# Kernel tuning notes

Hardware: AMD Instinct MI355X
Metric: run time of the kernel (lower is better)

The kernel has to match this reference:

```python
import jax, jax.numpy as jnp
import numpy as np

def setup_inputs() -> dict:
    key = jax.random.key(0)
    ks = jax.random.split(key, 8)
    B, n, in_dim, h = 4, 512, 300, 128
    word_vecs = jax.random.normal(ks[0], (B, n, in_dim), dtype=jnp.float32)
    mask = jnp.zeros((B, n, h), dtype=jnp.float32)
    s_in = 1.0 / np.sqrt(in_dim)
    s_h = 1.0 / np.sqrt(h)
    Wx_w = jax.random.normal(ks[1], (h, in_dim), dtype=jnp.float32) * s_in
    Wx_b = jnp.zeros((h,), dtype=jnp.float32)
    Wa_w = jax.random.normal(ks[2], (h, h), dtype=jnp.float32) * s_h
    Wa_b = jnp.zeros((h,), dtype=jnp.float32)
    Ua_w = jax.random.normal(ks[3], (h, h), dtype=jnp.float32) * s_h
    Ua_b = jnp.zeros((h,), dtype=jnp.float32)
    return {"word_vecs": word_vecs, "mask": mask, "Wx_w": Wx_w, "Wx_b": Wx_b,
            "Wa_w": Wa_w, "Wa_b": Wa_b, "Ua_w": Ua_w, "Ua_b": Ua_b}

def reference(word_vecs, mask, Wx_w, Wx_b, Wa_w, Wa_b, Ua_w, Ua_b):
    # h_vecs: [B, n, h]  (dropout layers are identity in eval mode)
    h_vecs = jnp.tanh(jnp.einsum('bni,hi->bnh', word_vecs, Wx_w) + Wx_b)
    ta = jnp.einsum('bnh,gh->bng', h_vecs, Wa_w) + Wa_b  # [B,n,h]
    tb = jnp.einsum('bnh,gh->bng', h_vecs, Ua_w) + Ua_b  # [B,n,h]
    # additive per-channel scores: [B, q, k, h]
    temp = jax.nn.elu(ta[:, :, None, :] + tb[:, None, :, :])
    a = jax.nn.softmax(temp + mask[:, None, :, :], axis=2)
    # weighted sum over keys: [B, q, h]
    c_vecs = jnp.einsum('bqkh,bkh->bqh', a, h_vecs)
    return c_vecs
```

## Files before the change

kernel.cpp:

```cpp
#include <hip/hip_runtime.h>

#define B_    4
#define N_    512
#define IND_  300
#define H_    128
#define QQ    8
#define KC    8
#define LOG2E 1.4426950408889634f

__global__ void pack_all(const float* __restrict__ Wx_w,
                         const float* __restrict__ Wa_w,
                         const float* __restrict__ Ua_w,
                         float* __restrict__ WxT4,
                         float* __restrict__ WaT4,
                         float* __restrict__ UaT4) {
    const int blk = blockIdx.x;
    const int t   = threadIdx.x;
    if (blk < IND_) {
        const int i = blk;
        WxT4[(i >> 2) * 512 + t * 4 + (i & 3)] = Wx_w[t * IND_ + i];
    } else if (blk < IND_ + H_) {
        const int i = blk - IND_;
        WaT4[(i >> 2) * 512 + t * 4 + (i & 3)] = Wa_w[t * H_ + i] * LOG2E;
    } else {
        const int i = blk - IND_ - H_;
        UaT4[(i >> 2) * 512 + t * 4 + (i & 3)] = Ua_w[t * H_ + i] * LOG2E;
    }
}

__global__ __launch_bounds__(128) void prep3(
    const float* __restrict__ x,
    const float* __restrict__ WxT4,
    const float* __restrict__ Wx_b,
    const float* __restrict__ WaT4,
    const float* __restrict__ Wa_b,
    const float* __restrict__ UaT4,
    const float* __restrict__ Ua_b,
    const float* __restrict__ mask,
    float* __restrict__ Eta,
    float4* __restrict__ kv)
{
    __shared__ __align__(16) float xs[304];
    __shared__ __align__(16) float hs[H_];

    const int r = blockIdx.x;
    const int t = threadIdx.x;

    const float* xrow = x + (size_t)r * IND_;
    for (int i = t; i < IND_; i += 128) xs[i] = xrow[i];
    __syncthreads();

    const float4* w4 = (const float4*)WxT4 + t;
    float acc = Wx_b[t];
    #pragma unroll 5
    for (int i4 = 0; i4 < IND_ / 4; ++i4) {
        float4 w  = w4[i4 * 128];
        float4 xv = *(const float4*)(xs + 4 * i4);
        acc = fmaf(w.x, xv.x, acc);
        acc = fmaf(w.y, xv.y, acc);
        acc = fmaf(w.z, xv.z, acc);
        acc = fmaf(w.w, xv.w, acc);
    }
    float h = tanhf(acc);
    hs[t] = h;
    __syncthreads();

    const float4* wa4 = (const float4*)WaT4 + t;
    const float4* ua4 = (const float4*)UaT4 + t;
    float accA = Wa_b[t] * LOG2E;
    float accU = Ua_b[t] * LOG2E;
    #pragma unroll 8
    for (int i4 = 0; i4 < H_ / 4; ++i4) {
        float4 wa = wa4[i4 * 128];
        float4 ua = ua4[i4 * 128];
        float4 hv = *(const float4*)(hs + 4 * i4);
        accA = fmaf(wa.x, hv.x, accA);
        accA = fmaf(wa.y, hv.y, accA);
        accA = fmaf(wa.z, hv.z, accA);
        accA = fmaf(wa.w, hv.w, accA);
        accU = fmaf(ua.x, hv.x, accU);
        accU = fmaf(ua.y, hv.y, accU);
        accU = fmaf(ua.z, hv.z, accU);
        accU = fmaf(ua.w, hv.w, accU);
    }
    const size_t o = (size_t)r * H_ + t;
    Eta[o] = __builtin_amdgcn_exp2f(accA);
    float M = __builtin_amdgcn_exp2f(mask[o] * LOG2E);
    kv[o]  = make_float4(__builtin_amdgcn_exp2f(accU), M, h, 0.f);
}

__global__ __launch_bounds__(128) void attn3(
    const float* __restrict__ Eta,
    const float4* __restrict__ kv,
    float2* __restrict__ accum)
{
    const int c  = blockIdx.x;
    const int qg = blockIdx.y;
    const int b  = blockIdx.z;
    const int h  = threadIdx.x;
    const int q0 = qg * QQ;
    const int k0 = c * (N_ / KC);

    float eta[QQ], l[QQ], cc[QQ];
    #pragma unroll
    for (int j = 0; j < QQ; ++j) {
        eta[j] = Eta[((size_t)(b * N_ + q0 + j)) * H_ + h];
        l[j] = 0.f;
        cc[j] = 0.f;
    }

    const float4* kp = kv + ((size_t)(b * N_ + k0)) * H_ + h;

    #pragma unroll 4
    for (int k = 0; k < N_ / KC; ++k) {
        float4 v = kp[(size_t)k * H_];
        #pragma unroll
        for (int j = 0; j < QQ; ++j) {
            float e  = eta[j] * v.x;
            float pn = __builtin_amdgcn_exp2f(fmaf(e, LOG2E, -LOG2E));
            float p0 = (e > 1.f) ? e : pn;
            float p  = p0 * v.y;
            l[j] += p;
            cc[j] = fmaf(p, v.z, cc[j]);
        }
    }

    #pragma unroll
    for (int j = 0; j < QQ; ++j) {
        accum[((size_t)c * (B_ * N_) + b * N_ + q0 + j) * H_ + h] =
            make_float2(l[j], cc[j]);
    }
}

__global__ void fin3(const float2* __restrict__ accum, float* __restrict__ out) {
    const int idx = blockIdx.x * 256 + threadIdx.x;
    float L = 0.f, C = 0.f;
    #pragma unroll
    for (int c = 0; c < KC; ++c) {
        float2 a = accum[(size_t)c * (B_ * N_ * H_) + idx];
        L += a.x;
        C += a.y;
    }
    out[idx] = C / L;
}

extern "C" void kernel_launch(void* const* d_in, const int* in_sizes, int n_in,
                              void* d_out, int out_size, void* d_ws, size_t ws_size,
                              hipStream_t stream) {
    const float* word_vecs = (const float*)d_in[0];
    const float* mask      = (const float*)d_in[1];
    const float* Wx_w      = (const float*)d_in[2];
    const float* Wx_b      = (const float*)d_in[3];
    const float* Wa_w      = (const float*)d_in[4];
    const float* Wa_b      = (const float*)d_in[5];
    const float* Ua_w      = (const float*)d_in[6];
    const float* Ua_b      = (const float*)d_in[7];
    float* out = (float*)d_out;

    char* p = (char*)d_ws;
    float*  WxT4  = (float*)p;   p += (size_t)75 * 512 * 4;
    float*  WaT4  = (float*)p;   p += (size_t)32 * 512 * 4;
    float*  UaT4  = (float*)p;   p += (size_t)32 * 512 * 4;
    float*  Eta   = (float*)p;   p += (size_t)B_ * N_ * H_ * 4;
    float4* kv    = (float4*)p;  p += (size_t)B_ * N_ * H_ * 16;
    float2* accum = (float2*)p;  p += (size_t)KC * B_ * N_ * H_ * 8;

    pack_all<<<IND_ + 2 * H_, 128, 0, stream>>>(Wx_w, Wa_w, Ua_w, WxT4, WaT4, UaT4);

    prep3<<<B_ * N_, 128, 0, stream>>>(word_vecs, WxT4, Wx_b,
                                       WaT4, Wa_b, UaT4, Ua_b,
                                       mask, Eta, kv);

    dim3 grid(KC, N_ / QQ, B_);
    attn3<<<grid, 128, 0, stream>>>(Eta, kv, accum);

    fin3<<<(B_ * N_ * H_) / 256, 256, 0, stream>>>(accum, out);
}
```

Measured before the change: 131.4 us.

## Process four rows per prep block, split keys finer, premultiply mask into values

The projection kernel now computes four rows per block, so each weight load is reused across rows and the x tile is loaded with float4. The key dimension is split into 16 chunks instead of 8 to create more attention blocks. The mask factor is folded into the stored value (M*h), so the inner loop uses two FMAs instead of a multiply plus add and FMA. The cost is a partial-sum buffer twice as large and more reduction traffic in the final kernel.

```diff
diff --git a/kernel.cpp b/kernel.cpp
--- a/kernel.cpp
+++ b/kernel.cpp
@@ -5,7 +5,8 @@
 #define IND_  300
 #define H_    128
 #define QQ    8
-#define KC    8
+#define KC    16
+#define RR    4
 #define LOG2E 1.4426950408889634f
 
 __global__ void pack_all(const float* __restrict__ Wx_w,
@@ -28,7 +29,7 @@
     }
 }
 
-__global__ __launch_bounds__(128) void prep3(
+__global__ __launch_bounds__(128) void prep4(
     const float* __restrict__ x,
     const float* __restrict__ WxT4,
     const float* __restrict__ Wx_b,
@@ -40,56 +41,78 @@
     float* __restrict__ Eta,
     float4* __restrict__ kv)
 {
-    __shared__ __align__(16) float xs[304];
-    __shared__ __align__(16) float hs[H_];
-
-    const int r = blockIdx.x;
-    const int t = threadIdx.x;
-
-    const float* xrow = x + (size_t)r * IND_;
-    for (int i = t; i < IND_; i += 128) xs[i] = xrow[i];
+    __shared__ __align__(16) float xs[RR * IND_];
+    __shared__ __align__(16) float hs[RR][H_];
+
+    const int r0 = blockIdx.x * RR;
+    const int t  = threadIdx.x;
+
+    const float4* xg = (const float4*)(x + (size_t)r0 * IND_);
+    float4* xs4 = (float4*)xs;
+    #pragma unroll
+    for (int i = t; i < RR * IND_ / 4; i += 128) xs4[i] = xg[i];
     __syncthreads();
 
+    float acc[RR];
+    {
+        const float bx = Wx_b[t];
+        #pragma unroll
+        for (int r = 0; r < RR; ++r) acc[r] = bx;
+    }
     const float4* w4 = (const float4*)WxT4 + t;
-    float acc = Wx_b[t];
     #pragma unroll 5
     for (int i4 = 0; i4 < IND_ / 4; ++i4) {
-        float4 w  = w4[i4 * 128];
-        float4 xv = *(const float4*)(xs + 4 * i4);
-        acc = fmaf(w.x, xv.x, acc);
-        acc = fmaf(w.y, xv.y, acc);
-        acc = fmaf(w.z, xv.z, acc);
-        acc = fmaf(w.w, xv.w, acc);
-    }
-    float h = tanhf(acc);
-    hs[t] = h;
+        float4 w = w4[i4 * 128];
+        #pragma unroll
+        for (int r = 0; r < RR; ++r) {
+            float4 xv = *(const float4*)(xs + r * IND_ + 4 * i4);
+            acc[r] = fmaf(w.x, xv.x, acc[r]);
+            acc[r] = fmaf(w.y, xv.y, acc[r]);
+            acc[r] = fmaf(w.z, xv.z, acc[r]);
+            acc[r] = fmaf(w.w, xv.w, acc[r]);
+        }
+    }
+    #pragma unroll
+    for (int r = 0; r < RR; ++r) hs[r][t] = tanhf(acc[r]);
     __syncthreads();
 
+    float accA[RR], accU[RR];
+    {
+        const float ba = Wa_b[t] * LOG2E;
+        const float bu = Ua_b[t] * LOG2E;
+        #pragma unroll
+        for (int r = 0; r < RR; ++r) { accA[r] = ba; accU[r] = bu; }
+    }
     const float4* wa4 = (const float4*)WaT4 + t;
     const float4* ua4 = (const float4*)UaT4 + t;
-    float accA = Wa_b[t] * LOG2E;
-    float accU = Ua_b[t] * LOG2E;
-    #pragma unroll 8
+    #pragma unroll 4
     for (int i4 = 0; i4 < H_ / 4; ++i4) {
         float4 wa = wa4[i4 * 128];
         float4 ua = ua4[i4 * 128];
-        float4 hv = *(const float4*)(hs + 4 * i4);
-        accA = fmaf(wa.x, hv.x, accA);
-        accA = fmaf(wa.y, hv.y, accA);
-        accA = fmaf(wa.z, hv.z, accA);
-        accA = fmaf(wa.w, hv.w, accA);
-        accU = fmaf(ua.x, hv.x, accU);
-        accU = fmaf(ua.y, hv.y, accU);
-        accU = fmaf(ua.z, hv.z, accU);
-        accU = fmaf(ua.w, hv.w, accU);
-    }
-    const size_t o = (size_t)r * H_ + t;
-    Eta[o] = __builtin_amdgcn_exp2f(accA);
-    float M = __builtin_amdgcn_exp2f(mask[o] * LOG2E);
-    kv[o]  = make_float4(__builtin_amdgcn_exp2f(accU), M, h, 0.f);
-}
-
-__global__ __launch_bounds__(128) void attn3(
+        #pragma unroll
+        for (int r = 0; r < RR; ++r) {
+            float4 hv = *(const float4*)(&hs[r][4 * i4]);
+            accA[r] = fmaf(wa.x, hv.x, accA[r]);
+            accA[r] = fmaf(wa.y, hv.y, accA[r]);
+            accA[r] = fmaf(wa.z, hv.z, accA[r]);
+            accA[r] = fmaf(wa.w, hv.w, accA[r]);
+            accU[r] = fmaf(ua.x, hv.x, accU[r]);
+            accU[r] = fmaf(ua.y, hv.y, accU[r]);
+            accU[r] = fmaf(ua.z, hv.z, accU[r]);
+            accU[r] = fmaf(ua.w, hv.w, accU[r]);
+        }
+    }
+    #pragma unroll
+    for (int r = 0; r < RR; ++r) {
+        const size_t o = (size_t)(r0 + r) * H_ + t;
+        Eta[o]  = __builtin_amdgcn_exp2f(accA[r]);
+        float M = __builtin_amdgcn_exp2f(mask[o] * LOG2E);
+        float h = hs[r][t];
+        kv[o]   = make_float4(__builtin_amdgcn_exp2f(accU[r]), M, M * h, 0.f);
+    }
+}
+
+__global__ __launch_bounds__(128) void attn4(
     const float* __restrict__ Eta,
     const float4* __restrict__ kv,
     float2* __restrict__ accum)
@@ -119,9 +142,8 @@
             float e  = eta[j] * v.x;
             float pn = __builtin_amdgcn_exp2f(fmaf(e, LOG2E, -LOG2E));
             float p0 = (e > 1.f) ? e : pn;
-            float p  = p0 * v.y;
-            l[j] += p;
-            cc[j] = fmaf(p, v.z, cc[j]);
+            l[j]  = fmaf(p0, v.y, l[j]);
+            cc[j] = fmaf(p0, v.z, cc[j]);
         }
     }
 
@@ -132,7 +154,7 @@
     }
 }
 
-__global__ void fin3(const float2* __restrict__ accum, float* __restrict__ out) {
+__global__ void fin4(const float2* __restrict__ accum, float* __restrict__ out) {
     const int idx = blockIdx.x * 256 + threadIdx.x;
     float L = 0.f, C = 0.f;
     #pragma unroll
@@ -167,12 +189,12 @@
 
     pack_all<<<IND_ + 2 * H_, 128, 0, stream>>>(Wx_w, Wa_w, Ua_w, WxT4, WaT4, UaT4);
 
-    prep3<<<B_ * N_, 128, 0, stream>>>(word_vecs, WxT4, Wx_b,
-                                       WaT4, Wa_b, UaT4, Ua_b,
-                                       mask, Eta, kv);
+    prep4<<<(B_ * N_) / RR, 128, 0, stream>>>(word_vecs, WxT4, Wx_b,
+                                              WaT4, Wa_b, UaT4, Ua_b,
+                                              mask, Eta, kv);
 
     dim3 grid(KC, N_ / QQ, B_);
-    attn3<<<grid, 128, 0, stream>>>(Eta, kv, accum);
-
-    fin3<<<(B_ * N_ * H_) / 256, 256, 0, stream>>>(accum, out);
-}
+    attn4<<<grid, 128, 0, stream>>>(Eta, kv, accum);
+
+    fin4<<<(B_ * N_ * H_) / 256, 256, 0, stream>>>(accum, out);
+}
```

Result: slower. 136.8 us (+4.0%).
